# Kernel optimization log

Measured on AMD Instinct MI355X. Metric: run time of the kernel, lower is better.

Reference implementation:

```python
import jax, jax.numpy as jnp
import numpy as np

N = 12288
E = 393216
H = 128
NEG = -1000000000.0

def setup_inputs() -> dict:
    key = jax.random.key(0)
    k1, k2, k3, k4, k5, k6 = jax.random.split(key, 6)
    h = jax.random.normal(k1, (N, H), dtype=jnp.float32)
    sources = jax.random.randint(k2, (E,), 0, N, dtype=jnp.int32)
    dests = jax.random.randint(k3, (E,), 0, N, dtype=jnp.int32)
    weights = jax.random.normal(k4, (E, 1), dtype=jnp.float32)
    # nn.Linear(2*H+1, 1) params
    W = jax.random.normal(k5, (1, 2 * H + 1), dtype=jnp.float32) / np.sqrt(2 * H + 1)
    b = jax.random.normal(k6, (1,), dtype=jnp.float32) * 0.01
    return {"h": h, "sources": sources, "dests": dests, "weights": weights, "W": W, "b": b}

def reference(h, sources, dests, weights, W, b):
    n = h.shape[0]
    # gather endpoint features and concat with edge weights: [E, 2H+1]
    edge_input = jnp.concatenate([h[dests], h[sources], weights], axis=1)
    vals = (edge_input @ W.T + b)[:, 0]  # [E]
    scores = jnp.full((n, n), NEG, dtype=h.dtype)
    scores = scores.at[dests, sources].set(vals)
    return scores
```

## Files before the change

### kernel.cpp

```cpp
#include <hip/hip_runtime.h>

#define NEG_VAL -1000000000.0f
#define MAXDEG  192
#define SEGF    1024


__global__ __launch_bounds__(256) void fill_and_dots(
    float4* __restrict__ out4, long long n4, int fillBlocks,
    const float* __restrict__ h, const float* __restrict__ W,
    float* __restrict__ a, float* __restrict__ c, int N)
{
    if ((int)blockIdx.x < fillBlocks) {
        long long i = (long long)blockIdx.x * 256 + threadIdx.x;
        if (i < n4) out4[i] = make_float4(NEG_VAL, NEG_VAL, NEG_VAL, NEG_VAL);
    } else {
        int gid  = (blockIdx.x - fillBlocks) * 256 + threadIdx.x;
        int node = gid >> 6;
        int lane = threadIdx.x & 63;
        if (node >= N) return;
        const float2* h2 = (const float2*)(h + (size_t)node * 128);
        float2 v  = h2[lane];
        float2 wd = ((const float2*)W)[lane];
        float2 ws = ((const float2*)(W + 128))[lane];
        float sd = v.x * wd.x + v.y * wd.y;
        float ss = v.x * ws.x + v.y * ws.y;
        #pragma unroll
        for (int off = 32; off; off >>= 1) {
            sd += __shfl_xor(sd, off, 64);
            ss += __shfl_xor(ss, off, 64);
        }
        if (lane == 0) { a[node] = sd; c[node] = ss; }
    }
}

__global__ __launch_bounds__(256) void edge_scatter(
    const int* __restrict__ src, const int* __restrict__ dst,
    const float* __restrict__ wgt, const float* __restrict__ a,
    const float* __restrict__ c, const float* __restrict__ W,
    const float* __restrict__ b, float* __restrict__ out, int E, int N)
{
    int e = blockIdx.x * blockDim.x + threadIdx.x;
    if (e >= E) return;
    int s = src[e];
    int d = dst[e];
    out[(size_t)d * N + s] = fmaf(wgt[e], W[256], a[d] + c[s] + b[0]);
}


__global__ __launch_bounds__(256) void zero_cursor(int* __restrict__ cursor, int N) {
    int i = blockIdx.x * 256 + threadIdx.x;
    if (i < N) cursor[i] = 0;
}

__global__ __launch_bounds__(256) void dots_and_emit(
    const float* __restrict__ h, const float* __restrict__ W,
    float* __restrict__ a, float* __restrict__ c, int N,
    const int* __restrict__ src, const int* __restrict__ dst,
    const float* __restrict__ wgt,
    int* __restrict__ cursor, int2* __restrict__ csr, int E, int dotBlocks)
{
    if ((int)blockIdx.x < dotBlocks) {
        int gid  = blockIdx.x * 256 + threadIdx.x;
        int node = gid >> 6;
        int lane = threadIdx.x & 63;
        if (node >= N) return;
        const float2* h2 = (const float2*)(h + (size_t)node * 128);
        float2 v  = h2[lane];
        float2 wd = ((const float2*)W)[lane];
        float2 ws = ((const float2*)(W + 128))[lane];
        float sd = v.x * wd.x + v.y * wd.y;
        float ss = v.x * ws.x + v.y * ws.y;
        #pragma unroll
        for (int off = 32; off; off >>= 1) {
            sd += __shfl_xor(sd, off, 64);
            ss += __shfl_xor(ss, off, 64);
        }
        if (lane == 0) { a[node] = sd; c[node] = ss; }
    } else {
        int e = (blockIdx.x - dotBlocks) * 256 + threadIdx.x;
        if (e >= E) return;
        int d = dst[e];
        int slot = atomicAdd(&cursor[d], 1);
        if (slot < MAXDEG)
            csr[(size_t)d * MAXDEG + slot] = make_int2(src[e], __float_as_int(wgt[e]));
    }
}

__global__ __launch_bounds__(256) void fill_patch(
    float4* __restrict__ out4,
    const float* __restrict__ a, const float* __restrict__ c,
    const int* __restrict__ cursor, const int2* __restrict__ csr,
    const float* __restrict__ W, const float* __restrict__ b, int N)
{
    __shared__ int   pcol[256];
    __shared__ float pval[256];
    __shared__ int   pcnt;

    int seg        = blockIdx.x;
    int segsPerRow = N >> 10;
    int r          = seg / segsPerRow;
    int colBase    = (seg - r * segsPerRow) << 10;
    int tid        = threadIdx.x;

    if (tid == 0) pcnt = 0;
    __syncthreads();

    int   cnt  = min(cursor[r], MAXDEG);
    float w256 = W[256];
    float bb   = b[0];
    float ar   = a[r];

    for (int i = tid; i < cnt; i += 256) {
        int2 eo  = csr[(size_t)r * MAXDEG + i];
        int  rel = eo.x - colBase;
        if ((unsigned)rel < SEGF) {
            int k = atomicAdd(&pcnt, 1);
            if (k < 256) {
                pcol[k] = rel;
                pval[k] = fmaf(__int_as_float(eo.y), w256, ar + c[eo.x] + bb);
            }
        }
    }
    __syncthreads();

    float4 v = make_float4(NEG_VAL, NEG_VAL, NEG_VAL, NEG_VAL);
    int m = min(pcnt, 256);
    for (int k = 0; k < m; ++k) {
        int rel = pcol[k];
        if ((rel >> 2) == tid) ((float*)&v)[rel & 3] = pval[k];
    }
    out4[(size_t)seg * (SEGF / 4) + tid] = v;
}

extern "C" void kernel_launch(void* const* d_in, const int* in_sizes, int n_in,
                              void* d_out, int out_size, void* d_ws, size_t ws_size,
                              hipStream_t stream) {
    const float* h       = (const float*)d_in[0];
    const int*   sources = (const int*)d_in[1];
    const int*   dests   = (const int*)d_in[2];
    const float* weights = (const float*)d_in[3];
    const float* W       = (const float*)d_in[4];
    const float* b       = (const float*)d_in[5];
    float* out = (float*)d_out;

    const int N = in_sizes[0] / 128;
    const int E = in_sizes[1];

    float* a      = (float*)d_ws;
    float* c      = a + N;
    int*   cursor = (int*)(c + N);
    int2*  csr    = (int2*)(cursor + N);
    size_t wsNeed = (size_t)N * 12 + (size_t)N * MAXDEG * 8;

    if ((N % 1024) == 0 && ws_size >= wsNeed) {
        zero_cursor<<<(N + 255) / 256, 256, 0, stream>>>(cursor, N);

        int dotBlocks  = N / 4;
        int emitBlocks = (E + 255) / 256;
        dots_and_emit<<<dotBlocks + emitBlocks, 256, 0, stream>>>(
            h, W, a, c, N, sources, dests, weights, cursor, csr, E, dotBlocks);

        int nseg = (N >> 10) * N;
        fill_patch<<<nseg, 256, 0, stream>>>(
            (float4*)out, a, c, cursor, csr, W, b, N);
    } else {
        long long n4 = (long long)out_size / 4;
        int fillBlocks = (int)((n4 + 255) / 256);
        int dotBlocks  = (N + 3) / 4;
        fill_and_dots<<<fillBlocks + dotBlocks, 256, 0, stream>>>(
            (float4*)out, n4, fillBlocks, h, W, a, c, N);
        int blocks = (E + 255) / 256;
        edge_scatter<<<blocks, 256, 0, stream>>>(sources, dests, weights, a, c, W, b,
                                                 out, E, N);
    }
}
```

Baseline: 714.1 us.

## Shrink per-row edge buckets, add overflow list, write patches directly

Per-row edge bucket capacity drops from 192 to 128 slots, and edges beyond that spill into a global overflow list that every fill block scans. The fill kernel now writes the NEG float4 tile first and then scatters edge values straight to global memory, one bucket slot per thread. This removes the shared-memory atomics and the serial per-thread search loop. It also reduces CSR footprint, at the cost of an extra global overflow count read per block, plus the risk that write ordering between the fill store and the scattered stores within a block relies on __syncthreads visibility.

```diff
diff --git a/kernel.cpp b/kernel.cpp
--- a/kernel.cpp
+++ b/kernel.cpp
@@ -1,7 +1,8 @@
 #include <hip/hip_runtime.h>
 
 #define NEG_VAL -1000000000.0f
-#define MAXDEG  192
+#define MAXDEG  128
+#define OVFCAP  4096
 #define SEGF    1024
 
 
@@ -47,9 +48,11 @@
 }
 
 
-__global__ __launch_bounds__(256) void zero_cursor(int* __restrict__ cursor, int N) {
+__global__ __launch_bounds__(256) void zero_meta(int* __restrict__ cursor, int N,
+                                                 int* __restrict__ ovf_cnt) {
     int i = blockIdx.x * 256 + threadIdx.x;
     if (i < N) cursor[i] = 0;
+    if (i == 0) *ovf_cnt = 0;
 }
 
 __global__ __launch_bounds__(256) void dots_and_emit(
@@ -57,7 +60,9 @@
     float* __restrict__ a, float* __restrict__ c, int N,
     const int* __restrict__ src, const int* __restrict__ dst,
     const float* __restrict__ wgt,
-    int* __restrict__ cursor, int2* __restrict__ csr, int E, int dotBlocks)
+    int* __restrict__ cursor, int2* __restrict__ csr,
+    int4* __restrict__ ovf, int* __restrict__ ovf_cnt,
+    int E, int dotBlocks)
 {
     if ((int)blockIdx.x < dotBlocks) {
         int gid  = blockIdx.x * 256 + threadIdx.x;
@@ -80,56 +85,68 @@
         int e = (blockIdx.x - dotBlocks) * 256 + threadIdx.x;
         if (e >= E) return;
         int d = dst[e];
+        int s = src[e];
+        int wbits = __float_as_int(wgt[e]);
         int slot = atomicAdd(&cursor[d], 1);
-        if (slot < MAXDEG)
-            csr[(size_t)d * MAXDEG + slot] = make_int2(src[e], __float_as_int(wgt[e]));
+        if (slot < MAXDEG) {
+            csr[(size_t)d * MAXDEG + slot] = make_int2(s, wbits);
+        } else {
+            int k = atomicAdd(ovf_cnt, 1);
+            if (k < OVFCAP) ovf[k] = make_int4(d, s, wbits, 0);
+        }
     }
 }
 
 __global__ __launch_bounds__(256) void fill_patch(
-    float4* __restrict__ out4,
+    float* __restrict__ out,
     const float* __restrict__ a, const float* __restrict__ c,
     const int* __restrict__ cursor, const int2* __restrict__ csr,
-    const float* __restrict__ W, const float* __restrict__ b, int N)
+    const int4* __restrict__ ovf, const int* __restrict__ ovf_cnt,
+    const float* __restrict__ W, const float* __restrict__ b,
+    int segsPerRow)
 {
-    __shared__ int   pcol[256];
-    __shared__ float pval[256];
-    __shared__ int   pcnt;
+    int seg = blockIdx.x;
+    int tid = threadIdx.x;
+    int r   = seg / segsPerRow;
+    int colBase = (seg - r * segsPerRow) << 10;
 
-    int seg        = blockIdx.x;
-    int segsPerRow = N >> 10;
-    int r          = seg / segsPerRow;
-    int colBase    = (seg - r * segsPerRow) << 10;
-    int tid        = threadIdx.x;
+    float4* out4 = (float4*)out + (size_t)seg * (SEGF / 4);
+    out4[tid] = make_float4(NEG_VAL, NEG_VAL, NEG_VAL, NEG_VAL);
 
-    if (tid == 0) pcnt = 0;
+    int cnt = cursor[r];
+    if (cnt > MAXDEG) cnt = MAXDEG;
+    int2  eo;
+    float ar = 0.f, w256 = 0.f, bb = 0.f, cs = 0.f;
+    int   rel = -1;
+    bool  mine = (tid < cnt);
+    if (mine) {
+        eo  = csr[(size_t)r * MAXDEG + tid];
+        rel = eo.x - colBase;
+        mine = ((unsigned)rel < SEGF);
+        if (mine) {
+            ar = a[r]; w256 = W[256]; bb = b[0]; cs = c[eo.x];
+        }
+    }
+    int no = *ovf_cnt;
+
     __syncthreads();
 
-    int   cnt  = min(cursor[r], MAXDEG);
-    float w256 = W[256];
-    float bb   = b[0];
-    float ar   = a[r];
-
-    for (int i = tid; i < cnt; i += 256) {
-        int2 eo  = csr[(size_t)r * MAXDEG + i];
-        int  rel = eo.x - colBase;
-        if ((unsigned)rel < SEGF) {
-            int k = atomicAdd(&pcnt, 1);
-            if (k < 256) {
-                pcol[k] = rel;
-                pval[k] = fmaf(__int_as_float(eo.y), w256, ar + c[eo.x] + bb);
+    if (mine) {
+        out[(size_t)seg * SEGF + rel] = fmaf(__int_as_float(eo.y), w256, ar + cs + bb);
+    }
+    if (no > 0) {
+        if (no > OVFCAP) no = OVFCAP;
+        for (int k = tid; k < no; k += 256) {
+            int4 o = ovf[k];
+            if (o.x == r) {
+                int rr = o.y - colBase;
+                if ((unsigned)rr < SEGF) {
+                    out[(size_t)seg * SEGF + rr] =
+                        fmaf(__int_as_float(o.z), W[256], a[r] + c[o.y] + b[0]);
+                }
             }
         }
     }
-    __syncthreads();
-
-    float4 v = make_float4(NEG_VAL, NEG_VAL, NEG_VAL, NEG_VAL);
-    int m = min(pcnt, 256);
-    for (int k = 0; k < m; ++k) {
-        int rel = pcol[k];
-        if ((rel >> 2) == tid) ((float*)&v)[rel & 3] = pval[k];
-    }
-    out4[(size_t)seg * (SEGF / 4) + tid] = v;
 }
 
 extern "C" void kernel_launch(void* const* d_in, const int* in_sizes, int n_in,
@@ -146,23 +163,27 @@
     const int N = in_sizes[0] / 128;
     const int E = in_sizes[1];
 
-    float* a      = (float*)d_ws;
-    float* c      = a + N;
-    int*   cursor = (int*)(c + N);
-    int2*  csr    = (int2*)(cursor + N);
-    size_t wsNeed = (size_t)N * 12 + (size_t)N * MAXDEG * 8;
+    float* a       = (float*)d_ws;
+    float* c       = a + N;
+    int*   cursor  = (int*)(c + N);
+    int4*  ovf     = (int4*)(cursor + N);
+    int*   ovf_cnt = (int*)(ovf + OVFCAP);
+    int2*  csr     = (int2*)(ovf_cnt + 4);
+    size_t wsNeed  = (size_t)N * 12 + (size_t)OVFCAP * 16 + 16 + (size_t)N * MAXDEG * 8;
 
-    if ((N % 1024) == 0 && ws_size >= wsNeed) {
-        zero_cursor<<<(N + 255) / 256, 256, 0, stream>>>(cursor, N);
+    if ((N % SEGF) == 0 && ws_size >= wsNeed) {
+        zero_meta<<<(N + 255) / 256, 256, 0, stream>>>(cursor, N, ovf_cnt);
 
         int dotBlocks  = N / 4;
         int emitBlocks = (E + 255) / 256;
         dots_and_emit<<<dotBlocks + emitBlocks, 256, 0, stream>>>(
-            h, W, a, c, N, sources, dests, weights, cursor, csr, E, dotBlocks);
+            h, W, a, c, N, sources, dests, weights, cursor, csr, ovf, ovf_cnt,
+            E, dotBlocks);
 
-        int nseg = (N >> 10) * N;
+        int segsPerRow = N / SEGF;
+        int nseg       = segsPerRow * N;
         fill_patch<<<nseg, 256, 0, stream>>>(
-            (float4*)out, a, c, cursor, csr, W, b, N);
+            out, a, c, cursor, csr, ovf, ovf_cnt, W, b, segsPerRow);
     } else {
         long long n4 = (long long)out_size / 4;
         int fillBlocks = (int)((n4 + 255) / 256);
```

Result: faster. 666.0 us (-6.7%).
